# Kernel tuning notes

Measured on AMD Instinct MI355X. Metric: run time of the kernel, lower is better.

The kernel has to match this reference:

```python
import jax, jax.numpy as jnp
import numpy as np

NU, NI, D, NNZ = 80000, 40000, 128, 2000000
EPS = 1e-12


def _spmm(dst, src, vals, x, n):
    # sum_e vals[e] * x[src[e]] scattered to dst[e]; A is [n, x.shape[0]] in COO.
    return jax.ops.segment_sum(vals[:, None] * x[src], dst, num_segments=n)


def setup_inputs() -> dict:
    key = jax.random.key(0)
    ks = jax.random.split(key, 24)
    limit = float(np.sqrt(6.0 / (D + D)))  # xavier_uniform
    inp = {
        'user_embedding': jax.random.normal(ks[0], (NU, D), jnp.float32),
        'item_embedding': jax.random.normal(ks[1], (NI, D), jnp.float32),
        'uu_embed0': jax.random.normal(ks[2], (NU, D), jnp.float32),
        'ii_embed0': jax.random.normal(ks[3], (NI, D), jnp.float32),
        'uu_embed1': jax.random.normal(ks[4], (NU, D), jnp.float32),
        'ii_embed1': jax.random.normal(ks[5], (NI, D), jnp.float32),
        'uu_embed2': jax.random.normal(ks[6], (NU, D), jnp.float32),
        'ii_embed2': jax.random.normal(ks[7], (NI, D), jnp.float32),
        'u_w': jax.random.uniform(ks[8], (D, D), jnp.float32, -limit, limit),
        'i_w': jax.random.uniform(ks[9], (D, D), jnp.float32, -limit, limit),
    }
    for b in range(4):
        inp[f'rows{b}'] = jax.random.randint(ks[10 + 3 * b], (NNZ,), 0, NU, jnp.int32)
        inp[f'cols{b}'] = jax.random.randint(ks[11 + 3 * b], (NNZ,), 0, NI, jnp.int32)
        inp[f'vals{b}'] = jax.random.uniform(ks[12 + 3 * b], (NNZ,), jnp.float32)
    return inp


def reference(user_embedding, item_embedding, uu_embed0, ii_embed0, uu_embed1,
              ii_embed1, uu_embed2, ii_embed2, u_w, i_w,
              rows0, cols0, vals0, rows1, cols1, vals1,
              rows2, cols2, vals2, rows3, cols3, vals3):
    nu, ni = user_embedding.shape[0], item_embedding.shape[0]
    # behavior 0 = click, 1 = fav, 2 = cart, 3 = buy
    u0 = _spmm(rows0, cols0, vals0, ii_embed0, nu)
    i0 = _spmm(cols0, rows0, vals0, uu_embed0, ni)
    u1 = _spmm(rows1, cols1, vals1, ii_embed1, nu)
    i1 = _spmm(cols1, rows1, vals1, uu_embed1, ni)
    u2 = _spmm(rows2, cols2, vals2, ii_embed2, nu)
    i2 = _spmm(cols2, rows2, vals2, uu_embed2, ni)
    u3 = _spmm(rows3, cols3, vals3, item_embedding, nu)
    i3 = _spmm(cols3, rows3, vals3, user_embedding, ni)
    user_embeddings = jnp.stack([u0, u1, u2, u3], axis=0)  # [4, NU, D]
    item_embeddings = jnp.stack([i0, i1, i2, i3], axis=0)  # [4, NI, D]
    user_out = jax.nn.sigmoid(jnp.mean(user_embeddings, axis=0) @ u_w)
    item_out = jax.nn.sigmoid(jnp.mean(item_embeddings, axis=0) @ i_w)
    # F.normalize default: L2 over dim=1 (the node axis of the stacked tensor)
    def l2n(x):
        return x / jnp.maximum(jnp.linalg.norm(x, axis=1, keepdims=True), EPS)
    return (user_out, item_out, l2n(user_embeddings), l2n(item_embeddings),
            u0, i0, u1, i1, u2, i2)
```

## Files before the change

### kernel.cpp

```cpp
#include <hip/hip_runtime.h>

#define NU 80000
#define NI 40000
#define DD 128
#define NNZ_E 2000000
#define EPSN 1e-12f
#define BWROWS 256
#define NBU 313
#define NBI 157
#define NBPAD 320
#define BSTRIDE 336
#define BIN_E 8192
#define S2CAP 16384
#define NREP 4
#define GF_NBU 2500
#define GF_NBI 1250

struct EdgePtrs { const int* rows[4]; const int* cols[4]; const float* vals[4]; };

struct GAll {
  const int* rp[2][4];
  const int2* pairs[2][4];
  const unsigned short* xt[2][4];
  float* out[2][4];
  float* dup[2][4];
  float* meanb[2];
  float* colsums;
};

struct ConvPtrs { const float* src[8]; unsigned short* dst[8]; int n4[8]; };

__device__ inline unsigned short f2bf(float f) {
  unsigned int u = __float_as_uint(f);
  u += 0x7FFFu + ((u >> 16) & 1u);
  return (unsigned short)(u >> 16);
}
__device__ inline float bf2f(unsigned short h) {
  return __uint_as_float((unsigned)h << 16);
}

__global__ __launch_bounds__(256) void convA_k(ConvPtrs cp) {
  int y = blockIdx.y;
  const float4* __restrict__ src = (const float4*)cp.src[y];
  ushort4* __restrict__ dst = (ushort4*)cp.dst[y];
  int n4 = cp.n4[y];
  int stride = blockDim.x * gridDim.x;
  for (int i = blockIdx.x * blockDim.x + threadIdx.x; i < n4; i += stride) {
    float4 f = src[i];
    ushort4 h;
    h.x = f2bf(f.x); h.y = f2bf(f.y); h.z = f2bf(f.z); h.w = f2bf(f.w);
    dst[i] = h;
  }
}

__global__ __launch_bounds__(256) void conv_k(const float* __restrict__ src,
                                              unsigned short* __restrict__ dst, int n4) {
  int stride = blockDim.x * gridDim.x;
  for (int i = blockIdx.x * blockDim.x + threadIdx.x; i < n4; i += stride) {
    float4 f = ((const float4*)src)[i];
    ushort4 h;
    h.x = f2bf(f.x); h.y = f2bf(f.y); h.z = f2bf(f.z); h.w = f2bf(f.w);
    ((ushort4*)dst)[i] = h;
  }
}

__global__ __launch_bounds__(256) void histB_k(EdgePtrs ep, int* cntA) {
  int b = blockIdx.y;
  const int* __restrict__ rows = ep.rows[b];
  const int* __restrict__ cols = ep.cols[b];
  __shared__ int lh[NBU + NBI];
  for (int i = threadIdx.x; i < NBU + NBI; i += blockDim.x) lh[i] = 0;
  __syncthreads();
  int stride = blockDim.x * gridDim.x;
  for (int e = blockIdx.x * blockDim.x + threadIdx.x; e < NNZ_E; e += stride) {
    atomicAdd(&lh[rows[e] >> 8], 1);
    atomicAdd(&lh[NBU + (cols[e] >> 8)], 1);
  }
  __syncthreads();
  int* cu = cntA + (b * 2 + 0) * NBPAD;
  int* ci = cntA + (b * 2 + 1) * NBPAD;
  for (int i = threadIdx.x; i < NBU + NBI; i += blockDim.x) {
    int v = lh[i];
    if (v) {
      if (i < NBU) atomicAdd(&cu[i], v);
      else atomicAdd(&ci[i - NBU], v);
    }
  }
}

__global__ __launch_bounds__(512) void scanb_k(const int* cntA, int* baseA, int* gcurA) {
  __shared__ int wsums[9];
  int a = blockIdx.x;
  int dir = a & 1;
  int n = dir ? NBI : NBU;
  const int* cnt = cntA + a * NBPAD;
  int* base = baseA + a * BSTRIDE;
  int* gcur = gcurA + a * NBPAD;
  int t = threadIdx.x, lane = t & 63, w = t >> 6;
  int v = (t < n) ? cnt[t] : 0;
  int s = v;
  #pragma unroll
  for (int off = 1; off < 64; off <<= 1) {
    int x = __shfl_up(s, off);
    if (lane >= off) s += x;
  }
  if (lane == 63) wsums[w] = s;
  __syncthreads();
  if (t == 0) {
    int run = 0;
    for (int k = 0; k < 8; k++) { int x = wsums[k]; wsums[k] = run; run += x; }
    wsums[8] = run;
  }
  __syncthreads();
  int ex = wsums[w] + s - v;
  if (t < n) { base[t] = ex; gcur[t] = ex; }
  if (t == 0) base[n] = wsums[8];
}

__global__ __launch_bounds__(512) void bin_k(EdgePtrs ep, int b0, int* gcurA, int2* binned) {
  __shared__ int2 stage[BIN_E];
  __shared__ int lh[NBPAD], lscan[NBPAD], lcur[NBPAD], gpos[NBPAD];
  __shared__ int wsums[9];
  int dir = blockIdx.y, j = blockIdx.z, b = b0 + j;
  int NB = dir ? NBI : NBU;
  const int* __restrict__ dst = dir ? ep.cols[b] : ep.rows[b];
  const int* __restrict__ src = dir ? ep.rows[b] : ep.cols[b];
  const float* __restrict__ vals = ep.vals[b];
  int* gcur = gcurA + (b * 2 + dir) * NBPAD;
  int2* out = binned + ((size_t)j * 2 + dir) * NNZ_E;
  int t = threadIdx.x;
  int e0 = blockIdx.x * BIN_E;
  int nh = min(BIN_E, NNZ_E - e0);
  for (int i = t; i < NBPAD; i += 512) lh[i] = 0;
  __syncthreads();
  for (int i = t; i < nh; i += 512) atomicAdd(&lh[dst[e0 + i] >> 8], 1);
  __syncthreads();
  {
    int lane = t & 63, w = t >> 6;
    int v = (t < NB) ? lh[t] : 0;
    int s = v;
    #pragma unroll
    for (int off = 1; off < 64; off <<= 1) {
      int x = __shfl_up(s, off);
      if (lane >= off) s += x;
    }
    if (lane == 63) wsums[w] = s;
    __syncthreads();
    if (t == 0) {
      int run = 0;
      for (int k = 0; k < 8; k++) { int x = wsums[k]; wsums[k] = run; run += x; }
      wsums[8] = run;
    }
    __syncthreads();
    int ex = wsums[w] + s - v;
    if (t < NB) { lscan[t] = ex; lcur[t] = ex; gpos[t] = atomicAdd(&gcur[t], v); }
  }
  __syncthreads();
  for (int i = t; i < nh; i += 512) {
    int d = dst[e0 + i], s = src[e0 + i];
    int k = d >> 8;
    int pos = atomicAdd(&lcur[k], 1);
    stage[pos] = make_int2(s | ((d & 255) << 17), __float_as_int(vals[e0 + i]));
  }
  __syncthreads();
  int w = t >> 6, lane = t & 63;
  for (int k = w; k < NB; k += 8) {
    int c = lh[k];
    const int2* sp = stage + lscan[k];
    int2* gp = out + gpos[k];
    for (int i = lane; i < c; i += 64) gp[i] = sp[i];
  }
}

__global__ __launch_bounds__(512) void sort3_k(int* rpU, int* rpI, int b0,
                                               const int* baseA, int2* binned) {
  __shared__ int2 stage[S2CAP];
  __shared__ int lh[256];
  __shared__ int excl[257];
  __shared__ int lcur[256];
  __shared__ int wsums[5];
  int gb = blockIdx.x;
  int j = gb / (NBU + NBI);
  int r = gb - j * (NBU + NBI);
  int dir = (r >= NBU) ? 1 : 0;
  int k = dir ? (r - NBU) : r;
  int b = b0 + j;
  int n = dir ? NI : NU;
  int* rp = dir ? (rpI + (size_t)b * (NI + 1)) : (rpU + (size_t)b * (NU + 1));
  const int* base = baseA + (b * 2 + dir) * BSTRIDE;
  int2* bb = binned + ((size_t)j * 2 + dir) * NNZ_E;
  int row0 = k << 8;
  int nrows = min(BWROWS, n - row0);
  int base0 = base[k];
  int tot = base[k + 1] - base0;
  int t = threadIdx.x;
  if (t < 256) lh[t] = 0;
  __syncthreads();
  for (int i = t; i < tot; i += 512) atomicAdd(&lh[(bb[base0 + i].x >> 17) & 255], 1);
  __syncthreads();
  int v = 0, s = 0;
  if (t < 256) {
    int lane = t & 63, w = t >> 6;
    v = lh[t]; s = v;
    #pragma unroll
    for (int off = 1; off < 64; off <<= 1) {
      int x = __shfl_up(s, off);
      if (lane >= off) s += x;
    }
    if (lane == 63) wsums[w] = s;
  }
  __syncthreads();
  if (t == 0) {
    int run = 0;
    for (int q = 0; q < 4; q++) { int x = wsums[q]; wsums[q] = run; run += x; }
    wsums[4] = run;
  }
  __syncthreads();
  if (t < 256) {
    int ex = wsums[t >> 6] + s - v;
    excl[t] = ex; lcur[t] = ex;
  }
  if (t == 0) excl[256] = wsums[4];
  __syncthreads();
  if (t <= nrows) rp[row0 + t] = base0 + excl[t];
  for (int i = t; i < tot; i += 512) {
    int2 p = bb[base0 + i];
    int ld = (p.x >> 17) & 255;
    int pos = atomicAdd(&lcur[ld], 1);
    stage[pos] = make_int2(p.x & 0x1FFFF, p.y);
  }
  __syncthreads();
  for (int i = t; i < tot; i += 512) bb[base0 + i] = stage[i];
}

__global__ __launch_bounds__(256) void gatherF_k(GAll g) {
  int blk = blockIdx.x;
  int dir = (blk >= GF_NBU) ? 1 : 0;
  int lblk = dir ? (blk - GF_NBU) : blk;
  int gid = lblk * 8 + (threadIdx.x >> 5);
  int lane = threadIdx.x & 31;
  int t = threadIdx.x;
  int r0 = gid * 4;

  float4 z = make_float4(0.f, 0.f, 0.f, 0.f);
  float4 mean[4] = {z, z, z, z};
  float4 sq[4] = {z, z, z, z};

  #pragma unroll
  for (int b = 0; b < 4; b++) {
    const int* __restrict__ rp = g.rp[dir][b];
    const int2* __restrict__ pairs = g.pairs[dir][b];
    const ushort4* __restrict__ x4 = (const ushort4*)g.xt[dir][b];
    float4* __restrict__ outp = (float4*)g.out[dir][b];
    float4* __restrict__ dupp = (float4*)g.dup[dir][b];
    #pragma unroll
    for (int k = 0; k < 4; k++) {
      int r = r0 + k;
      int beg = rp[r], end = rp[r + 1];
      float4 a0 = z, a1 = z;
      int e = beg;
      for (; e + 3 < end; e += 4) {
        int2 p0 = pairs[e], p1 = pairs[e + 1], p2 = pairs[e + 2], p3 = pairs[e + 3];
        ushort4 h0 = x4[(size_t)p0.x * 32 + lane];
        ushort4 h1 = x4[(size_t)p1.x * 32 + lane];
        ushort4 h2 = x4[(size_t)p2.x * 32 + lane];
        ushort4 h3 = x4[(size_t)p3.x * 32 + lane];
        float v0 = __int_as_float(p0.y), v1 = __int_as_float(p1.y);
        float v2 = __int_as_float(p2.y), v3 = __int_as_float(p3.y);
        a0.x += v0 * bf2f(h0.x); a0.y += v0 * bf2f(h0.y);
        a0.z += v0 * bf2f(h0.z); a0.w += v0 * bf2f(h0.w);
        a1.x += v1 * bf2f(h1.x); a1.y += v1 * bf2f(h1.y);
        a1.z += v1 * bf2f(h1.z); a1.w += v1 * bf2f(h1.w);
        a0.x += v2 * bf2f(h2.x); a0.y += v2 * bf2f(h2.y);
        a0.z += v2 * bf2f(h2.z); a0.w += v2 * bf2f(h2.w);
        a1.x += v3 * bf2f(h3.x); a1.y += v3 * bf2f(h3.y);
        a1.z += v3 * bf2f(h3.z); a1.w += v3 * bf2f(h3.w);
      }
      for (; e < end; e++) {
        int2 p = pairs[e];
        ushort4 h = x4[(size_t)p.x * 32 + lane];
        float v = __int_as_float(p.y);
        a0.x += v * bf2f(h.x); a0.y += v * bf2f(h.y);
        a0.z += v * bf2f(h.z); a0.w += v * bf2f(h.w);
      }
      float4 res = make_float4(a0.x + a1.x, a0.y + a1.y, a0.z + a1.z, a0.w + a1.w);
      outp[(size_t)r * 32 + lane] = res;
      if (dupp) dupp[(size_t)r * 32 + lane] = res;
      mean[k].x += res.x; mean[k].y += res.y; mean[k].z += res.z; mean[k].w += res.w;
      sq[b].x += res.x * res.x; sq[b].y += res.y * res.y;
      sq[b].z += res.z * res.z; sq[b].w += res.w * res.w;
    }
  }
  float4* mb = (float4*)g.meanb[dir];
  #pragma unroll
  for (int k = 0; k < 4; k++) {
    float4 m = mean[k];
    m.x *= 0.25f; m.y *= 0.25f; m.z *= 0.25f; m.w *= 0.25f;
    mb[(size_t)(r0 + k) * 32 + lane] = m;
  }
  __shared__ float csq[512];
  csq[t] = 0.f; csq[t + 256] = 0.f;
  __syncthreads();
  int cb = lane * 4;
  #pragma unroll
  for (int b = 0; b < 4; b++) {
    atomicAdd(&csq[b * 128 + cb + 0], sq[b].x);
    atomicAdd(&csq[b * 128 + cb + 1], sq[b].y);
    atomicAdd(&csq[b * 128 + cb + 2], sq[b].z);
    atomicAdd(&csq[b * 128 + cb + 3], sq[b].w);
  }
  __syncthreads();
  float* dst = g.colsums + (blockIdx.x & (NREP - 1)) * 1024 + dir * 512;
  atomicAdd(&dst[t], csq[t]);
  atomicAdd(&dst[t + 256], csq[t + 256]);
}

__global__ __launch_bounds__(256) void gather_k(const int* __restrict__ rp, const int2* __restrict__ pairs,
                                                const void* __restrict__ xt, int isbf,
                                                float* __restrict__ out1, float* __restrict__ out2,
                                                int nrows) {
  int gid = blockIdx.x * 8 + (threadIdx.x >> 5);
  int lane = threadIdx.x & 31;
  int tot = gridDim.x * 8;
  for (int r = gid; r < nrows; r += tot) {
    int beg = rp[r], end = rp[r + 1];
    float4 a0 = make_float4(0.f, 0.f, 0.f, 0.f);
    int e = beg;
    if (isbf) {
      const ushort4* __restrict__ x4 = (const ushort4*)xt;
      for (; e < end; e++) {
        int2 p = pairs[e];
        ushort4 h = x4[(size_t)p.x * 32 + lane];
        float v = __int_as_float(p.y);
        a0.x += v * bf2f(h.x); a0.y += v * bf2f(h.y);
        a0.z += v * bf2f(h.z); a0.w += v * bf2f(h.w);
      }
    } else {
      const float4* __restrict__ x4 = (const float4*)xt;
      for (; e < end; e++) {
        int2 p = pairs[e];
        float4 xv = x4[(size_t)p.x * 32 + lane];
        float v = __int_as_float(p.y);
        a0.x += v * xv.x; a0.y += v * xv.y; a0.z += v * xv.z; a0.w += v * xv.w;
      }
    }
    ((float4*)out1)[(size_t)r * 32 + lane] = a0;
    if (out2) ((float4*)out2)[(size_t)r * 32 + lane] = a0;
  }
}

__global__ __launch_bounds__(256) void gemm2_k(const float* __restrict__ meanU,
                                               const float* __restrict__ meanI,
                                               const float* __restrict__ u_w,
                                               const float* __restrict__ i_w,
                                               float* __restrict__ user_out,
                                               float* __restrict__ item_out) {
  __shared__ float wl[DD * DD];
  __shared__ float rl[8][DD];
  int blk = blockIdx.x;
  const float* mean; const float* W; float* outp; int n; int row0;
  if (blk < NU / 64) { mean = meanU; W = u_w; outp = user_out; n = NU; row0 = blk * 64; }
  else { mean = meanI; W = i_w; outp = item_out; n = NI; row0 = (blk - NU / 64) * 64; }
  for (int i = threadIdx.x; i < DD * DD / 4; i += blockDim.x)
    ((float4*)wl)[i] = ((const float4*)W)[i];
  int c = threadIdx.x & 127;
  int g = threadIdx.x >> 7;
  for (int rr = 0; rr < 64; rr += 8) {
    int rbase = row0 + rr;
    __syncthreads();
    for (int i = threadIdx.x; i < 8 * DD; i += blockDim.x) {
      int lr = i >> 7, lc = i & 127;
      int r = rbase + lr;
      rl[lr][lc] = (r < n) ? mean[(size_t)r * DD + lc] : 0.f;
    }
    __syncthreads();
    float acc0 = 0.f, acc1 = 0.f, acc2 = 0.f, acc3 = 0.f;
    #pragma unroll 4
    for (int k = 0; k < DD; k++) {
      float wv = wl[k * DD + c];
      acc0 += rl[g * 4 + 0][k] * wv;
      acc1 += rl[g * 4 + 1][k] * wv;
      acc2 += rl[g * 4 + 2][k] * wv;
      acc3 += rl[g * 4 + 3][k] * wv;
    }
    float accs[4] = {acc0, acc1, acc2, acc3};
    for (int jj = 0; jj < 4; jj++) {
      int r = rbase + g * 4 + jj;
      if (r < n) outp[(size_t)r * DD + c] = 1.f / (1.f + __expf(-accs[jj]));
    }
  }
}

__global__ __launch_bounds__(256) void gemm_sig_k(const float* __restrict__ x, size_t sstride,
                                                  const float* __restrict__ W, float* __restrict__ out,
                                                  int n) {
  __shared__ float wl[DD * DD];
  __shared__ float rl[8][DD];
  for (int i = threadIdx.x; i < DD * DD / 4; i += blockDim.x)
    ((float4*)wl)[i] = ((const float4*)W)[i];
  int c = threadIdx.x & 127;
  int g = threadIdx.x >> 7;
  int row0 = blockIdx.x * 64;
  for (int rr = 0; rr < 64; rr += 8) {
    int rbase = row0 + rr;
    __syncthreads();
    for (int i = threadIdx.x; i < 8 * DD; i += blockDim.x) {
      int lr = i >> 7, lc = i & 127;
      int r = rbase + lr;
      float m = 0.f;
      if (r < n) {
        size_t off = (size_t)r * DD + lc;
        m = 0.25f * (x[off] + x[off + sstride] + x[off + 2 * sstride] + x[off + 3 * sstride]);
      }
      rl[lr][lc] = m;
    }
    __syncthreads();
    float acc0 = 0.f, acc1 = 0.f, acc2 = 0.f, acc3 = 0.f;
    #pragma unroll 4
    for (int k = 0; k < DD; k++) {
      float wv = wl[k * DD + c];
      acc0 += rl[g * 4 + 0][k] * wv;
      acc1 += rl[g * 4 + 1][k] * wv;
      acc2 += rl[g * 4 + 2][k] * wv;
      acc3 += rl[g * 4 + 3][k] * wv;
    }
    float accs[4] = {acc0, acc1, acc2, acc3};
    for (int jj = 0; jj < 4; jj++) {
      int r = rbase + g * 4 + jj;
      if (r < n) out[(size_t)r * DD + c] = 1.f / (1.f + __expf(-accs[jj]));
    }
  }
}

__global__ __launch_bounds__(256) void colsq_k(const float* __restrict__ base, size_t sstride, int n,
                                               float* __restrict__ sums) {
  int b = blockIdx.y;
  const float* x = base + (size_t)b * sstride;
  int c = threadIdx.x & 127;
  int rh = threadIdx.x >> 7;
  float acc = 0.f;
  for (int r = blockIdx.x * 2 + rh; r < n; r += gridDim.x * 2) {
    float v = x[(size_t)r * DD + c];
    acc += v * v;
  }
  __shared__ float red[256];
  red[threadIdx.x] = acc;
  __syncthreads();
  if (threadIdx.x < 128) atomicAdd(&sums[b * DD + threadIdx.x], red[threadIdx.x] + red[threadIdx.x + 128]);
}

__global__ void inv_k(const float* __restrict__ sums, float* __restrict__ inv, int n, int nrep) {
  int i = blockIdx.x * blockDim.x + threadIdx.x;
  if (i < n) {
    float s = 0.f;
    for (int r = 0; r < nrep; r++) s += sums[r * 1024 + i];
    inv[i] = 1.f / fmaxf(sqrtf(s), EPSN);
  }
}

__global__ __launch_bounds__(256) void scaleall2_k(float* __restrict__ l2nU, float* __restrict__ l2nI,
                                                   const float* __restrict__ colsums) {
  __shared__ float sinv[DD];
  int y = blockIdx.y;
  int t = threadIdx.x;
  if (t < DD) {
    float s = 0.f;
    #pragma unroll
    for (int rr = 0; rr < NREP; rr++) s += colsums[rr * 1024 + y * DD + t];
    sinv[t] = 1.f / fmaxf(sqrtf(s), EPSN);
  }
  __syncthreads();
  float4* b4;
  size_t slice;
  if (y < 4) { b4 = (float4*)l2nU + (size_t)y * NU * 32; slice = (size_t)NU * 32; }
  else { b4 = (float4*)l2nI + (size_t)(y - 4) * NI * 32; slice = (size_t)NI * 32; }
  const float4* inv4 = (const float4*)sinv;
  size_t stride = (size_t)blockDim.x * gridDim.x;
  for (size_t i = (size_t)blockIdx.x * blockDim.x + threadIdx.x; i < slice; i += stride) {
    float4 s = inv4[i & 31];
    float4 v = b4[i];
    v.x *= s.x; v.y *= s.y; v.z *= s.z; v.w *= s.w;
    b4[i] = v;
  }
}

__global__ __launch_bounds__(256) void scaleall_k(float* __restrict__ l2nU, float* __restrict__ l2nI,
                                                  const float* __restrict__ invs) {
  int y = blockIdx.y;
  float4* b4;
  size_t slice;
  if (y < 4) { b4 = (float4*)l2nU + (size_t)y * NU * 32; slice = (size_t)NU * 32; }
  else { b4 = (float4*)l2nI + (size_t)(y - 4) * NI * 32; slice = (size_t)NI * 32; }
  const float4* inv4 = (const float4*)invs + (size_t)y * 32;
  size_t stride = (size_t)blockDim.x * gridDim.x;
  for (size_t i = (size_t)blockIdx.x * blockDim.x + threadIdx.x; i < slice; i += stride) {
    float4 s = inv4[i & 31];
    float4 v = b4[i];
    v.x *= s.x; v.y *= s.y; v.z *= s.z; v.w *= s.w;
    b4[i] = v;
  }
}

extern "C" void kernel_launch(void* const* d_in, const int* in_sizes, int n_in,
                              void* d_out, int out_size, void* d_ws, size_t ws_size,
                              hipStream_t stream) {
  const float* user_emb = (const float*)d_in[0];
  const float* item_emb = (const float*)d_in[1];
  const float* uu[4] = {(const float*)d_in[2], (const float*)d_in[4], (const float*)d_in[6], user_emb};
  const float* ii[4] = {(const float*)d_in[3], (const float*)d_in[5], (const float*)d_in[7], item_emb};
  const float* u_w = (const float*)d_in[8];
  const float* i_w = (const float*)d_in[9];
  EdgePtrs ep;
  for (int b = 0; b < 4; b++) {
    ep.rows[b] = (const int*)d_in[10 + 3 * b];
    ep.cols[b] = (const int*)d_in[11 + 3 * b];
    ep.vals[b] = (const float*)d_in[12 + 3 * b];
  }

  float* out = (float*)d_out;
  float* user_out = out;
  float* item_out = out + (size_t)NU * DD;
  float* l2nU = item_out + (size_t)NI * DD;
  float* l2nI = l2nU + (size_t)4 * NU * DD;
  float* u_slot[3];
  float* i_slot[3];
  {
    float* p = l2nI + (size_t)4 * NI * DD;
    for (int b = 0; b < 3; b++) {
      u_slot[b] = p; p += (size_t)NU * DD;
      i_slot[b] = p; p += (size_t)NI * DD;
    }
  }

  const size_t binsl = (size_t)2 * NNZ_E * 8;
  const size_t item_bf_sz = (size_t)4 * NI * DD * 2;
  const size_t user_bf_sz = (size_t)4 * NU * DD * 2;
  const size_t mean_sz = (size_t)(NU + NI) * DD * 4;
  const size_t smalls = 8u << 20;

  int batchB; bool bfI, bfU;
  if (ws_size >= 4 * binsl + item_bf_sz + user_bf_sz + mean_sz + smalls) { batchB = 4; bfI = bfU = true; }
  else if (ws_size >= 2 * binsl + item_bf_sz + user_bf_sz + smalls) { batchB = 2; bfI = bfU = true; }
  else if (ws_size >= binsl + item_bf_sz + user_bf_sz + smalls) { batchB = 1; bfI = bfU = true; }
  else if (ws_size >= binsl + item_bf_sz + smalls) { batchB = 1; bfI = true; bfU = false; }
  else { batchB = 1; bfI = bfU = false; }

  char* w = (char*)d_ws;
  auto alloc = [&](size_t bytes) {
    char* r = w;
    w += (bytes + 255) & ~(size_t)255;
    return r;
  };
  int2* binned = (int2*)alloc((size_t)batchB * binsl);
  unsigned short* itemB = bfI ? (unsigned short*)alloc(item_bf_sz) : nullptr;
  unsigned short* userB = bfU ? (unsigned short*)alloc(user_bf_sz) : nullptr;
  float* meanU = nullptr;
  float* meanI = nullptr;
  if (batchB == 4) {
    meanU = (float*)alloc((size_t)NU * DD * 4);
    meanI = (float*)alloc((size_t)NI * DD * 4);
  }
  int* cntA = (int*)alloc(4 * 2 * NBPAD * 4);
  int* baseA = (int*)alloc(4 * 2 * BSTRIDE * 4);
  int* gcurA = (int*)alloc(4 * 2 * NBPAD * 4);
  int* rpU = (int*)alloc((size_t)4 * (NU + 1) * 4);
  int* rpI = (int*)alloc((size_t)4 * (NI + 1) * 4);
  float* colsums = (float*)alloc(NREP * 1024 * 4);
  float* invs = (float*)alloc(8 * DD * 4);

  hipMemsetAsync(cntA, 0, 4 * 2 * NBPAD * 4, stream);
  histB_k<<<dim3(256, 4), 256, 0, stream>>>(ep, cntA);
  scanb_k<<<8, 512, 0, stream>>>(cntA, baseA, gcurA);

  const int nchunks = (NNZ_E + BIN_E - 1) / BIN_E;

  if (batchB == 4) {
    bin_k<<<dim3(nchunks, 2, 4), 512, 0, stream>>>(ep, 0, gcurA, binned);
    sort3_k<<<4 * (NBU + NBI), 512, 0, stream>>>(rpU, rpI, 0, baseA, binned);

    ConvPtrs cp;
    for (int b = 0; b < 4; b++) {
      cp.src[b] = ii[b]; cp.dst[b] = itemB + (size_t)b * NI * DD; cp.n4[b] = NI * DD / 4;
      cp.src[4 + b] = uu[b]; cp.dst[4 + b] = userB + (size_t)b * NU * DD; cp.n4[4 + b] = NU * DD / 4;
    }
    convA_k<<<dim3(512, 8), 256, 0, stream>>>(cp);
    hipMemsetAsync(colsums, 0, NREP * 1024 * 4, stream);

    GAll g;
    for (int b = 0; b < 4; b++) {
      g.rp[0][b] = rpU + (size_t)b * (NU + 1);
      g.pairs[0][b] = binned + ((size_t)b * 2 + 0) * NNZ_E;
      g.xt[0][b] = itemB + (size_t)b * NI * DD;
      g.out[0][b] = l2nU + (size_t)b * NU * DD;
      g.dup[0][b] = (b < 3) ? u_slot[b] : nullptr;
      g.rp[1][b] = rpI + (size_t)b * (NI + 1);
      g.pairs[1][b] = binned + ((size_t)b * 2 + 1) * NNZ_E;
      g.xt[1][b] = userB + (size_t)b * NU * DD;
      g.out[1][b] = l2nI + (size_t)b * NI * DD;
      g.dup[1][b] = (b < 3) ? i_slot[b] : nullptr;
    }
    g.meanb[0] = meanU; g.meanb[1] = meanI;
    g.colsums = colsums;
    gatherF_k<<<GF_NBU + GF_NBI, 256, 0, stream>>>(g);

    gemm2_k<<<NU / 64 + NI / 64, 256, 0, stream>>>(meanU, meanI, u_w, i_w, user_out, item_out);
    scaleall2_k<<<dim3(1024, 8), 256, 0, stream>>>(l2nU, l2nI, colsums);
  } else {
    if (bfI)
      for (int b = 0; b < 4; b++)
        conv_k<<<512, 256, 0, stream>>>(ii[b], itemB + (size_t)b * NI * DD, NI * DD / 4);
    if (bfU)
      for (int b = 0; b < 4; b++)
        conv_k<<<512, 256, 0, stream>>>(uu[b], userB + (size_t)b * NU * DD, NU * DD / 4);
    for (int b0 = 0; b0 < 4; b0 += batchB) {
      bin_k<<<dim3(nchunks, 2, batchB), 512, 0, stream>>>(ep, b0, gcurA, binned);
      sort3_k<<<batchB * (NBU + NBI), 512, 0, stream>>>(rpU, rpI, b0, baseA, binned);
      for (int j = 0; j < batchB; j++) {
        int b = b0 + j;
        const void* xt0 = bfI ? (const void*)(itemB + (size_t)b * NI * DD) : (const void*)ii[b];
        const void* xt1 = bfU ? (const void*)(userB + (size_t)b * NU * DD) : (const void*)uu[b];
        gather_k<<<10000, 256, 0, stream>>>(rpU + (size_t)b * (NU + 1),
                                            binned + ((size_t)j * 2 + 0) * NNZ_E, xt0, bfI ? 1 : 0,
                                            l2nU + (size_t)b * NU * DD, (b < 3) ? u_slot[b] : nullptr, NU);
        gather_k<<<5000, 256, 0, stream>>>(rpI + (size_t)b * (NI + 1),
                                           binned + ((size_t)j * 2 + 1) * NNZ_E, xt1, bfU ? 1 : 0,
                                           l2nI + (size_t)b * NI * DD, (b < 3) ? i_slot[b] : nullptr, NI);
      }
    }
    gemm_sig_k<<<NU / 64, 256, 0, stream>>>(l2nU, (size_t)NU * DD, u_w, user_out, NU);
    gemm_sig_k<<<NI / 64, 256, 0, stream>>>(l2nI, (size_t)NI * DD, i_w, item_out, NI);
    hipMemsetAsync(colsums, 0, NREP * 1024 * 4, stream);
    colsq_k<<<dim3(512, 4), 256, 0, stream>>>(l2nU, (size_t)NU * DD, NU, colsums);
    colsq_k<<<dim3(512, 4), 256, 0, stream>>>(l2nI, (size_t)NI * DD, NI, colsums + 4 * DD);
    inv_k<<<4, 256, 0, stream>>>(colsums, invs, 8 * DD, 1);
    scaleall_k<<<dim3(1024, 8), 256, 0, stream>>>(l2nU, l2nI, invs);
  }
}
```

Measured before the change: 1.422 ms.

## Move duplicate output writes into scale pass, deepen gather unroll, use nontemporal stores

```diff
diff --git a/kernel.cpp b/kernel.cpp
--- a/kernel.cpp
+++ b/kernel.cpp
@@ -13,8 +13,6 @@
 #define BIN_E 8192
 #define S2CAP 16384
 #define NREP 4
-#define GF_NBU 2500
-#define GF_NBI 1250
 
 struct EdgePtrs { const int* rows[4]; const int* cols[4]; const float* vals[4]; };
 
@@ -23,12 +21,19 @@
   const int2* pairs[2][4];
   const unsigned short* xt[2][4];
   float* out[2][4];
-  float* dup[2][4];
   float* meanb[2];
   float* colsums;
 };
 
+struct DupPtrs { float* d[8]; };
+
 struct ConvPtrs { const float* src[8]; unsigned short* dst[8]; int n4[8]; };
+
+typedef float f32x4 __attribute__((ext_vector_type(4)));
+__device__ inline void nts(float4 v, float4* p) {
+  f32x4 w = {v.x, v.y, v.z, v.w};
+  __builtin_nontemporal_store(w, (f32x4*)p);
+}
 
 __device__ inline unsigned short f2bf(float f) {
   unsigned int u = __float_as_uint(f);
@@ -233,11 +238,8 @@
   for (int i = t; i < tot; i += 512) bb[base0 + i] = stage[i];
 }
 
-__global__ __launch_bounds__(256) void gatherF_k(GAll g) {
-  int blk = blockIdx.x;
-  int dir = (blk >= GF_NBU) ? 1 : 0;
-  int lblk = dir ? (blk - GF_NBU) : blk;
-  int gid = lblk * 8 + (threadIdx.x >> 5);
+__global__ __launch_bounds__(256) void gatherD_k(GAll g, int dir) {
+  int gid = blockIdx.x * 8 + (threadIdx.x >> 5);
   int lane = threadIdx.x & 31;
   int t = threadIdx.x;
   int r0 = gid * 4;
@@ -252,29 +254,30 @@
     const int2* __restrict__ pairs = g.pairs[dir][b];
     const ushort4* __restrict__ x4 = (const ushort4*)g.xt[dir][b];
     float4* __restrict__ outp = (float4*)g.out[dir][b];
-    float4* __restrict__ dupp = (float4*)g.dup[dir][b];
     #pragma unroll
     for (int k = 0; k < 4; k++) {
       int r = r0 + k;
       int beg = rp[r], end = rp[r + 1];
       float4 a0 = z, a1 = z;
       int e = beg;
-      for (; e + 3 < end; e += 4) {
-        int2 p0 = pairs[e], p1 = pairs[e + 1], p2 = pairs[e + 2], p3 = pairs[e + 3];
-        ushort4 h0 = x4[(size_t)p0.x * 32 + lane];
-        ushort4 h1 = x4[(size_t)p1.x * 32 + lane];
-        ushort4 h2 = x4[(size_t)p2.x * 32 + lane];
-        ushort4 h3 = x4[(size_t)p3.x * 32 + lane];
-        float v0 = __int_as_float(p0.y), v1 = __int_as_float(p1.y);
-        float v2 = __int_as_float(p2.y), v3 = __int_as_float(p3.y);
-        a0.x += v0 * bf2f(h0.x); a0.y += v0 * bf2f(h0.y);
-        a0.z += v0 * bf2f(h0.z); a0.w += v0 * bf2f(h0.w);
-        a1.x += v1 * bf2f(h1.x); a1.y += v1 * bf2f(h1.y);
-        a1.z += v1 * bf2f(h1.z); a1.w += v1 * bf2f(h1.w);
-        a0.x += v2 * bf2f(h2.x); a0.y += v2 * bf2f(h2.y);
-        a0.z += v2 * bf2f(h2.z); a0.w += v2 * bf2f(h2.w);
-        a1.x += v3 * bf2f(h3.x); a1.y += v3 * bf2f(h3.y);
-        a1.z += v3 * bf2f(h3.z); a1.w += v3 * bf2f(h3.w);
+      for (; e + 8 <= end; e += 8) {
+        int2 pp[8];
+        ushort4 hh[8];
+        #pragma unroll
+        for (int q = 0; q < 8; q++) pp[q] = pairs[e + q];
+        #pragma unroll
+        for (int q = 0; q < 8; q++) hh[q] = x4[(size_t)pp[q].x * 32 + lane];
+        #pragma unroll
+        for (int q = 0; q < 8; q++) {
+          float v = __int_as_float(pp[q].y);
+          if (q & 1) {
+            a1.x += v * bf2f(hh[q].x); a1.y += v * bf2f(hh[q].y);
+            a1.z += v * bf2f(hh[q].z); a1.w += v * bf2f(hh[q].w);
+          } else {
+            a0.x += v * bf2f(hh[q].x); a0.y += v * bf2f(hh[q].y);
+            a0.z += v * bf2f(hh[q].z); a0.w += v * bf2f(hh[q].w);
+          }
+        }
       }
       for (; e < end; e++) {
         int2 p = pairs[e];
@@ -284,8 +287,7 @@
         a0.z += v * bf2f(h.z); a0.w += v * bf2f(h.w);
       }
       float4 res = make_float4(a0.x + a1.x, a0.y + a1.y, a0.z + a1.z, a0.w + a1.w);
-      outp[(size_t)r * 32 + lane] = res;
-      if (dupp) dupp[(size_t)r * 32 + lane] = res;
+      nts(res, (float4*)outp + (size_t)r * 32 + lane);
       mean[k].x += res.x; mean[k].y += res.y; mean[k].z += res.z; mean[k].w += res.w;
       sq[b].x += res.x * res.x; sq[b].y += res.y * res.y;
       sq[b].z += res.z * res.z; sq[b].w += res.w * res.w;
@@ -296,7 +298,7 @@
   for (int k = 0; k < 4; k++) {
     float4 m = mean[k];
     m.x *= 0.25f; m.y *= 0.25f; m.z *= 0.25f; m.w *= 0.25f;
-    mb[(size_t)(r0 + k) * 32 + lane] = m;
+    nts(m, mb + (size_t)(r0 + k) * 32 + lane);
   }
   __shared__ float csq[512];
   csq[t] = 0.f; csq[t + 256] = 0.f;
@@ -459,7 +461,7 @@
 }
 
 __global__ __launch_bounds__(256) void scaleall2_k(float* __restrict__ l2nU, float* __restrict__ l2nI,
-                                                   const float* __restrict__ colsums) {
+                                                   const float* __restrict__ colsums, DupPtrs dp) {
   __shared__ float sinv[DD];
   int y = blockIdx.y;
   int t = threadIdx.x;
@@ -474,13 +476,15 @@
   size_t slice;
   if (y < 4) { b4 = (float4*)l2nU + (size_t)y * NU * 32; slice = (size_t)NU * 32; }
   else { b4 = (float4*)l2nI + (size_t)(y - 4) * NI * 32; slice = (size_t)NI * 32; }
+  float4* dupp = (float4*)dp.d[y];
   const float4* inv4 = (const float4*)sinv;
   size_t stride = (size_t)blockDim.x * gridDim.x;
   for (size_t i = (size_t)blockIdx.x * blockDim.x + threadIdx.x; i < slice; i += stride) {
     float4 s = inv4[i & 31];
     float4 v = b4[i];
+    if (dupp) nts(v, dupp + i);
     v.x *= s.x; v.y *= s.y; v.z *= s.z; v.w *= s.w;
-    b4[i] = v;
+    nts(v, b4 + i);
   }
 }
 
@@ -592,19 +596,24 @@
       g.pairs[0][b] = binned + ((size_t)b * 2 + 0) * NNZ_E;
       g.xt[0][b] = itemB + (size_t)b * NI * DD;
       g.out[0][b] = l2nU + (size_t)b * NU * DD;
-      g.dup[0][b] = (b < 3) ? u_slot[b] : nullptr;
       g.rp[1][b] = rpI + (size_t)b * (NI + 1);
       g.pairs[1][b] = binned + ((size_t)b * 2 + 1) * NNZ_E;
       g.xt[1][b] = userB + (size_t)b * NU * DD;
       g.out[1][b] = l2nI + (size_t)b * NI * DD;
-      g.dup[1][b] = (b < 3) ? i_slot[b] : nullptr;
     }
     g.meanb[0] = meanU; g.meanb[1] = meanI;
     g.colsums = colsums;
-    gatherF_k<<<GF_NBU + GF_NBI, 256, 0, stream>>>(g);
+    gatherD_k<<<NU / 32, 256, 0, stream>>>(g, 0);
+    gatherD_k<<<NI / 32, 256, 0, stream>>>(g, 1);
 
     gemm2_k<<<NU / 64 + NI / 64, 256, 0, stream>>>(meanU, meanI, u_w, i_w, user_out, item_out);
-    scaleall2_k<<<dim3(1024, 8), 256, 0, stream>>>(l2nU, l2nI, colsums);
+
+    DupPtrs dp;
+    for (int b = 0; b < 4; b++) {
+      dp.d[b] = (b < 3) ? u_slot[b] : nullptr;
+      dp.d[4 + b] = (b < 3) ? i_slot[b] : nullptr;
+    }
+    scaleall2_k<<<dim3(1024, 8), 256, 0, stream>>>(l2nU, l2nI, colsums, dp);
   } else {
     if (bfI)
       for (int b = 0; b < 4; b++)
```

New measurement: 1.529 ms. 1.08x slower.

## Split fused gather by direction, move duplicate writes into scale pass, use nontemporal stores

Applied to the files above, without the earlier changes.

```diff
diff --git a/kernel.cpp b/kernel.cpp
--- a/kernel.cpp
+++ b/kernel.cpp
@@ -13,8 +13,6 @@
 #define BIN_E 8192
 #define S2CAP 16384
 #define NREP 4
-#define GF_NBU 2500
-#define GF_NBI 1250
 
 struct EdgePtrs { const int* rows[4]; const int* cols[4]; const float* vals[4]; };
 
@@ -23,12 +21,19 @@
   const int2* pairs[2][4];
   const unsigned short* xt[2][4];
   float* out[2][4];
-  float* dup[2][4];
   float* meanb[2];
   float* colsums;
 };
 
+struct DupPtrs { float* d[8]; };
+
 struct ConvPtrs { const float* src[8]; unsigned short* dst[8]; int n4[8]; };
+
+typedef float f32x4 __attribute__((ext_vector_type(4)));
+__device__ inline void nts(float4 v, float4* p) {
+  f32x4 w = {v.x, v.y, v.z, v.w};
+  __builtin_nontemporal_store(w, (f32x4*)p);
+}
 
 __device__ inline unsigned short f2bf(float f) {
   unsigned int u = __float_as_uint(f);
@@ -233,29 +238,19 @@
   for (int i = t; i < tot; i += 512) bb[base0 + i] = stage[i];
 }
 
-__global__ __launch_bounds__(256) void gatherF_k(GAll g) {
-  int blk = blockIdx.x;
-  int dir = (blk >= GF_NBU) ? 1 : 0;
-  int lblk = dir ? (blk - GF_NBU) : blk;
-  int gid = lblk * 8 + (threadIdx.x >> 5);
+__global__ __launch_bounds__(256) void gather4_k(GAll gm, int dir, int nrows, int ngroups) {
+  int gid = blockIdx.x * 8 + (threadIdx.x >> 5);
   int lane = threadIdx.x & 31;
   int t = threadIdx.x;
-  int r0 = gid * 4;
-
   float4 z = make_float4(0.f, 0.f, 0.f, 0.f);
-  float4 mean[4] = {z, z, z, z};
-  float4 sq[4] = {z, z, z, z};
-
-  #pragma unroll
-  for (int b = 0; b < 4; b++) {
-    const int* __restrict__ rp = g.rp[dir][b];
-    const int2* __restrict__ pairs = g.pairs[dir][b];
-    const ushort4* __restrict__ x4 = (const ushort4*)g.xt[dir][b];
-    float4* __restrict__ outp = (float4*)g.out[dir][b];
-    float4* __restrict__ dupp = (float4*)g.dup[dir][b];
+  float4 sq0 = z, sq1 = z, sq2 = z, sq3 = z;
+  for (int r = gid; r < nrows; r += ngroups) {
+    float4 mean = z;
     #pragma unroll
-    for (int k = 0; k < 4; k++) {
-      int r = r0 + k;
+    for (int b = 0; b < 4; b++) {
+      const int* rp = gm.rp[dir][b];
+      const int2* __restrict__ pairs = gm.pairs[dir][b];
+      const ushort4* __restrict__ x4 = (const ushort4*)gm.xt[dir][b];
       int beg = rp[r], end = rp[r + 1];
       float4 a0 = z, a1 = z;
       int e = beg;
@@ -284,33 +279,29 @@
         a0.z += v * bf2f(h.z); a0.w += v * bf2f(h.w);
       }
       float4 res = make_float4(a0.x + a1.x, a0.y + a1.y, a0.z + a1.z, a0.w + a1.w);
-      outp[(size_t)r * 32 + lane] = res;
-      if (dupp) dupp[(size_t)r * 32 + lane] = res;
-      mean[k].x += res.x; mean[k].y += res.y; mean[k].z += res.z; mean[k].w += res.w;
-      sq[b].x += res.x * res.x; sq[b].y += res.y * res.y;
-      sq[b].z += res.z * res.z; sq[b].w += res.w * res.w;
-    }
-  }
-  float4* mb = (float4*)g.meanb[dir];
-  #pragma unroll
-  for (int k = 0; k < 4; k++) {
-    float4 m = mean[k];
-    m.x *= 0.25f; m.y *= 0.25f; m.z *= 0.25f; m.w *= 0.25f;
-    mb[(size_t)(r0 + k) * 32 + lane] = m;
+      nts(res, (float4*)gm.out[dir][b] + (size_t)r * 32 + lane);
+      mean.x += res.x; mean.y += res.y; mean.z += res.z; mean.w += res.w;
+      float4* sqp = (b == 0) ? &sq0 : (b == 1) ? &sq1 : (b == 2) ? &sq2 : &sq3;
+      sqp->x += res.x * res.x; sqp->y += res.y * res.y;
+      sqp->z += res.z * res.z; sqp->w += res.w * res.w;
+    }
+    mean.x *= 0.25f; mean.y *= 0.25f; mean.z *= 0.25f; mean.w *= 0.25f;
+    ((float4*)gm.meanb[dir])[(size_t)r * 32 + lane] = mean;
   }
   __shared__ float csq[512];
   csq[t] = 0.f; csq[t + 256] = 0.f;
   __syncthreads();
   int cb = lane * 4;
-  #pragma unroll
-  for (int b = 0; b < 4; b++) {
-    atomicAdd(&csq[b * 128 + cb + 0], sq[b].x);
-    atomicAdd(&csq[b * 128 + cb + 1], sq[b].y);
-    atomicAdd(&csq[b * 128 + cb + 2], sq[b].z);
-    atomicAdd(&csq[b * 128 + cb + 3], sq[b].w);
-  }
-  __syncthreads();
-  float* dst = g.colsums + (blockIdx.x & (NREP - 1)) * 1024 + dir * 512;
+  atomicAdd(&csq[0 * 128 + cb + 0], sq0.x); atomicAdd(&csq[0 * 128 + cb + 1], sq0.y);
+  atomicAdd(&csq[0 * 128 + cb + 2], sq0.z); atomicAdd(&csq[0 * 128 + cb + 3], sq0.w);
+  atomicAdd(&csq[1 * 128 + cb + 0], sq1.x); atomicAdd(&csq[1 * 128 + cb + 1], sq1.y);
+  atomicAdd(&csq[1 * 128 + cb + 2], sq1.z); atomicAdd(&csq[1 * 128 + cb + 3], sq1.w);
+  atomicAdd(&csq[2 * 128 + cb + 0], sq2.x); atomicAdd(&csq[2 * 128 + cb + 1], sq2.y);
+  atomicAdd(&csq[2 * 128 + cb + 2], sq2.z); atomicAdd(&csq[2 * 128 + cb + 3], sq2.w);
+  atomicAdd(&csq[3 * 128 + cb + 0], sq3.x); atomicAdd(&csq[3 * 128 + cb + 1], sq3.y);
+  atomicAdd(&csq[3 * 128 + cb + 2], sq3.z); atomicAdd(&csq[3 * 128 + cb + 3], sq3.w);
+  __syncthreads();
+  float* dst = gm.colsums + (blockIdx.x & (NREP - 1)) * 1024 + dir * 512;
   atomicAdd(&dst[t], csq[t]);
   atomicAdd(&dst[t + 256], csq[t + 256]);
 }
@@ -459,7 +450,7 @@
 }
 
 __global__ __launch_bounds__(256) void scaleall2_k(float* __restrict__ l2nU, float* __restrict__ l2nI,
-                                                   const float* __restrict__ colsums) {
+                                                   const float* __restrict__ colsums, DupPtrs dp) {
   __shared__ float sinv[DD];
   int y = blockIdx.y;
   int t = threadIdx.x;
@@ -474,13 +465,15 @@
   size_t slice;
   if (y < 4) { b4 = (float4*)l2nU + (size_t)y * NU * 32; slice = (size_t)NU * 32; }
   else { b4 = (float4*)l2nI + (size_t)(y - 4) * NI * 32; slice = (size_t)NI * 32; }
+  float4* dupp = (float4*)dp.d[y];
   const float4* inv4 = (const float4*)sinv;
   size_t stride = (size_t)blockDim.x * gridDim.x;
   for (size_t i = (size_t)blockIdx.x * blockDim.x + threadIdx.x; i < slice; i += stride) {
     float4 s = inv4[i & 31];
     float4 v = b4[i];
+    if (dupp) nts(v, dupp + i);
     v.x *= s.x; v.y *= s.y; v.z *= s.z; v.w *= s.w;
-    b4[i] = v;
+    nts(v, b4 + i);
   }
 }
 
@@ -592,19 +585,24 @@
       g.pairs[0][b] = binned + ((size_t)b * 2 + 0) * NNZ_E;
       g.xt[0][b] = itemB + (size_t)b * NI * DD;
       g.out[0][b] = l2nU + (size_t)b * NU * DD;
-      g.dup[0][b] = (b < 3) ? u_slot[b] : nullptr;
       g.rp[1][b] = rpI + (size_t)b * (NI + 1);
       g.pairs[1][b] = binned + ((size_t)b * 2 + 1) * NNZ_E;
       g.xt[1][b] = userB + (size_t)b * NU * DD;
       g.out[1][b] = l2nI + (size_t)b * NI * DD;
-      g.dup[1][b] = (b < 3) ? i_slot[b] : nullptr;
     }
     g.meanb[0] = meanU; g.meanb[1] = meanI;
     g.colsums = colsums;
-    gatherF_k<<<GF_NBU + GF_NBI, 256, 0, stream>>>(g);
+    gather4_k<<<2500, 256, 0, stream>>>(g, 0, NU, 2500 * 8);
+    gather4_k<<<1250, 256, 0, stream>>>(g, 1, NI, 1250 * 8);
 
     gemm2_k<<<NU / 64 + NI / 64, 256, 0, stream>>>(meanU, meanI, u_w, i_w, user_out, item_out);
-    scaleall2_k<<<dim3(1024, 8), 256, 0, stream>>>(l2nU, l2nI, colsums);
+
+    DupPtrs dp;
+    for (int b = 0; b < 4; b++) {
+      dp.d[b] = (b < 3) ? u_slot[b] : nullptr;
+      dp.d[4 + b] = (b < 3) ? i_slot[b] : nullptr;
+    }
+    scaleall2_k<<<dim3(1024, 8), 256, 0, stream>>>(l2nU, l2nI, colsums, dp);
   } else {
     if (bfI)
       for (int b = 0; b < 4; b++)
```

Result: faster. 1.295 ms (median of 2 runs) (-8.9%).
